# Performance work log

Measured on AMD Instinct MI355X. Metric: run time of the kernel, lower is better.

The kernel has to match this reference:

```python
import jax, jax.numpy as jnp
import numpy as np

DIM = 256
HEADS = 8

def conv1x1(x, W, b):
    # x: [b,c,h,w], W: [o,c], b: [o]
    return jnp.einsum('oc,bchw->bohw', W, x) + b[None, :, None, None]

def setup_inputs() -> dict:
    key = jax.random.key(0)
    ks = jax.random.split(key, 16)
    B, C, H, Wd = 8, DIM, 96, 96
    s = 1.0 / np.sqrt(C)
    inp = {
        'x': jax.random.normal(ks[0], (B, C, H, Wd), jnp.float32),
        'y': jax.random.normal(ks[1], (B, C, H, Wd), jnp.float32),
        'z': jax.random.normal(ks[2], (B, C, H, Wd), jnp.float32),
        'W_qr': jax.random.normal(ks[3], (C // 2, C), jnp.float32) * s,
        'b_qr': jnp.zeros((C // 2,), jnp.float32),
        'W_qd': jax.random.normal(ks[4], (C // 2, C), jnp.float32) * s,
        'b_qd': jnp.zeros((C // 2,), jnp.float32),
        'W_kf': jax.random.normal(ks[5], (C, C), jnp.float32) * s,
        'b_kf': jnp.zeros((C,), jnp.float32),
        'W_vf': jax.random.normal(ks[6], (C, C), jnp.float32) * s,
        'b_vf': jnp.zeros((C,), jnp.float32),
        'W_cat': jax.random.normal(ks[7], (C, C), jnp.float32) * s,
        'b_cat': jnp.zeros((C,), jnp.float32),
        'W_proj': jax.random.normal(ks[8], (C, C), jnp.float32) * s,
        'b_proj': jnp.zeros((C,), jnp.float32),
        'temperature': jnp.ones((HEADS, 1, 1), jnp.float32),
    }
    return inp

def reference(x, y, z, W_qr, b_qr, W_qd, b_qd, W_kf, b_kf, W_vf, b_vf,
              W_cat, b_cat, W_proj, b_proj, temperature):
    b, c, h, w = x.shape
    hw = h * w
    ch = c // HEADS  # channels per head

    q_r = conv1x1(x, W_qr, b_qr)
    q_d = conv1x1(y, W_qd, b_qd)
    k_f = conv1x1(z, W_kf, b_kf)
    v_f = conv1x1(z, W_vf, b_vf)
    q = conv1x1(jnp.concatenate([q_r, q_d], axis=1), W_cat, b_cat)

    def to_heads(t):  # [b, head*ch, h, w] -> [b, head, ch, hw]
        return t.reshape(b, HEADS, ch, hw)

    q = to_heads(q)
    k = to_heads(k_f)
    v = to_heads(v_f)

    # L2-normalize along spatial axis (eps=1e-12 as in F.normalize)
    q = q / jnp.maximum(jnp.linalg.norm(q, axis=-1, keepdims=True), 1e-12)
    k = k / jnp.maximum(jnp.linalg.norm(k, axis=-1, keepdims=True), 1e-12)

    # channel attention: [b,head,ch,ch]
    attn = jnp.einsum('bhcn,bhdn->bhcd', q, k) * temperature[None]
    attn = jax.nn.softmax(attn, axis=-1)
    out = jnp.einsum('bhcd,bhdn->bhcn', attn, v)  # [b,head,ch,hw]
    out = out.reshape(b, c, h, w)
    return conv1x1(out, W_proj, b_proj) + z
```

## Files before the change

### kernel.cpp

```cpp
#include <hip/hip_runtime.h>

#define HW 9216
#define CDIM 256
#define NBATCH 8
#define NHEADS 8

typedef __bf16 bf16x8 __attribute__((ext_vector_type(8)));
typedef float f32x4 __attribute__((ext_vector_type(4)));
typedef float f32x2 __attribute__((ext_vector_type(2)));
typedef unsigned short us4v __attribute__((ext_vector_type(4)));
typedef unsigned short us2v __attribute__((ext_vector_type(2)));
typedef unsigned int u32x4 __attribute__((ext_vector_type(4)));

__device__ inline unsigned short f2bf(float f) {
    unsigned int u = __builtin_bit_cast(unsigned int, f);
    u = (u + 0x7FFF + ((u >> 16) & 1)) >> 16;
    return (unsigned short)u;
}
__device__ inline float bf2f(unsigned short s) {
    unsigned int u = ((unsigned int)s) << 16;
    return __builtin_bit_cast(float, u);
}
__device__ inline unsigned int pk2(float a, float b) {
    return (unsigned int)f2bf(a) | ((unsigned int)f2bf(b) << 16);
}
__device__ inline void stx(float* p, float v) { *p = v; }
__device__ inline void stx(unsigned short* p, float v) { *p = f2bf(v); }

__global__ void fuse_wq(const float* __restrict__ W_cat, const float* __restrict__ W_qr,
                        const float* __restrict__ W_qd, const float* __restrict__ b_qr,
                        const float* __restrict__ b_qd, const float* __restrict__ b_cat,
                        unsigned short* __restrict__ Wq, float* __restrict__ bq) {
    int o = blockIdx.x;
    int c = threadIdx.x;
    float ax = 0.f, ay = 0.f;
    for (int i = 0; i < 128; ++i) {
        ax += W_cat[o * 256 + i] * W_qr[i * 256 + c];
        ay += W_cat[o * 256 + 128 + i] * W_qd[i * 256 + c];
    }
    Wq[o * 512 + c] = f2bf(ax);
    Wq[o * 512 + 256 + c] = f2bf(ay);
    if (c == 0) {
        float s = b_cat[o];
        for (int i = 0; i < 128; ++i)
            s += W_cat[o * 256 + i] * b_qr[i] + W_cat[o * 256 + 128 + i] * b_qd[i];
        bq[o] = s;
    }
}

__global__ void cvt_w(const float* __restrict__ a, const float* __restrict__ b,
                      unsigned short* __restrict__ oa, unsigned short* __restrict__ ob) {
    int i = blockIdx.x * 256 + threadIdx.x;
    oa[i] = f2bf(a[i]);
    ob[i] = f2bf(b[i]);
}

template <int BN, bool DUAL, typename TX, typename TOut>
__global__ __launch_bounds__(256, 2) void gemm2(
    const unsigned short* __restrict__ A0, const unsigned short* __restrict__ A1,
    int a_bs, int Ktot,
    const TX* __restrict__ X0, const TX* __restrict__ X1,
    const float* __restrict__ bias0, const float* __restrict__ bias1,
    const float* __restrict__ resid, TOut* __restrict__ O0, TOut* __restrict__ O1) {
    constexpr int NJ = BN / 32;
    constexpr int NLD = (BN == 128) ? 4 : 2;
    constexpr int BUFB = 8 * BN * 16;

    const int b = blockIdx.z;
    const int n0 = blockIdx.x * BN;
    const int m0 = blockIdx.y * 128;
    const int tid = threadIdx.x;
    const int lane = tid & 63;
    const int wid = tid >> 6;
    const int wm = (wid >> 1) * 64;
    const int wn = (wid & 1) * (BN / 2);
    const int l15 = lane & 15;
    const int quad = lane >> 4;

    __shared__ __align__(16) char Bs[2][BUFB];

    const unsigned short* Ab0 = A0 + (size_t)b * a_bs;
    const unsigned short* Ab1 = DUAL ? A1 : nullptr;
    const TX* Xb0 = X0 + (size_t)b * CDIM * HW;
    const TX* Xb1 = X1 ? X1 + (size_t)b * CDIM * HW : nullptr;

    const int sn = (tid & 31) * NLD;
    const int so = (tid >> 5) * 8;

    f32x4 acc0[4][NJ] = {};
    f32x4 acc1[DUAL ? 4 : 1][NJ] = {};
    float f[8][NLD];

    auto LOADS = [&](int kg) {
        const TX* Xp = (Xb1 && kg >= 256) ? Xb1 : Xb0;
        const int kr = kg & 255;
#pragma unroll
        for (int r = 0; r < 8; ++r) {
            const TX* p = Xp + (size_t)(kr + so + r) * HW + n0 + sn;
            if constexpr (sizeof(TX) == 4) {
                if constexpr (NLD == 4) {
                    f32x4 v = *(const f32x4*)p;
#pragma unroll
                    for (int j = 0; j < 4; ++j) f[r][j] = v[j];
                } else {
                    f32x2 v = *(const f32x2*)p;
                    f[r][0] = v[0]; f[r][1] = v[1];
                }
            } else {
                if constexpr (NLD == 4) {
                    us4v v = *(const us4v*)p;
#pragma unroll
                    for (int j = 0; j < 4; ++j) f[r][j] = bf2f(v[j]);
                } else {
                    us2v v = *(const us2v*)p;
                    f[r][0] = bf2f(v[0]); f[r][1] = bf2f(v[1]);
                }
            }
        }
    };

    auto PKW = [&](int buf) {
        char* base = &Bs[buf][0];
#pragma unroll
        for (int j = 0; j < NLD; ++j) {
            int n = sn + j;
            u32x4 w;
            w[0] = pk2(f[0][j], f[1][j]);
            w[1] = pk2(f[2][j], f[3][j]);
            w[2] = pk2(f[4][j], f[5][j]);
            w[3] = pk2(f[6][j], f[7][j]);
            *(u32x4*)(base + ((((so >> 3) * BN + n) * 16) ^ ((n & 0x38) << 1))) = w;
        }
    };

    auto COMPUTE = [&](int buf, int k0) {
        const char* base = &Bs[buf][0];
#pragma unroll
        for (int kk = 0; kk < 64; kk += 32) {
            bf16x8 bfr[NJ];
#pragma unroll
            for (int nj = 0; nj < NJ; ++nj) {
                int n = wn + nj * 16 + l15;
                bfr[nj] = *(const bf16x8*)(base +
                    (((((kk >> 3) + quad) * BN + n) * 16) ^ ((n & 0x38) << 1)));
            }
            bf16x8 af[4];
#pragma unroll
            for (int mi = 0; mi < 4; ++mi)
                af[mi] = *(const bf16x8*)(Ab0 + (size_t)(m0 + wm + mi * 16 + l15) * Ktot +
                                          k0 + kk + quad * 8);
#pragma unroll
            for (int mi = 0; mi < 4; ++mi)
#pragma unroll
                for (int nj = 0; nj < NJ; ++nj)
                    acc0[mi][nj] = __builtin_amdgcn_mfma_f32_16x16x32_bf16(af[mi], bfr[nj],
                                                                           acc0[mi][nj], 0, 0, 0);
            if constexpr (DUAL) {
#pragma unroll
                for (int mi = 0; mi < 4; ++mi)
                    af[mi] = *(const bf16x8*)(Ab1 + (size_t)(m0 + wm + mi * 16 + l15) * Ktot +
                                              k0 + kk + quad * 8);
#pragma unroll
                for (int mi = 0; mi < 4; ++mi)
#pragma unroll
                    for (int nj = 0; nj < NJ; ++nj)
                        acc1[mi][nj] = __builtin_amdgcn_mfma_f32_16x16x32_bf16(af[mi], bfr[nj],
                                                                               acc1[mi][nj], 0, 0, 0);
            }
        }
    };

    const int nt = Ktot >> 6;
    LOADS(0);
    PKW(0);
    for (int t = 0; t < nt - 1; ++t) {
        LOADS((t + 1) << 6);
        __syncthreads();
        COMPUTE(t & 1, t << 6);
        PKW((t + 1) & 1);
    }
    __syncthreads();
    COMPUTE((nt - 1) & 1, (nt - 1) << 6);

#pragma unroll
    for (int mi = 0; mi < 4; ++mi) {
#pragma unroll
        for (int r = 0; r < 4; ++r) {
            int m = m0 + wm + mi * 16 + quad * 4 + r;
            float bv = bias0[m];
#pragma unroll
            for (int nj = 0; nj < NJ; ++nj) {
                int n = n0 + wn + nj * 16 + l15;
                size_t off = ((size_t)b * CDIM + m) * HW + n;
                float v = acc0[mi][nj][r] + bv;
                if (resid) v += resid[off];
                stx(&O0[off], v);
            }
        }
    }
    if constexpr (DUAL) {
#pragma unroll
        for (int mi = 0; mi < 4; ++mi) {
#pragma unroll
            for (int r = 0; r < 4; ++r) {
                int m = m0 + wm + mi * 16 + quad * 4 + r;
                float bv = bias1[m];
#pragma unroll
                for (int nj = 0; nj < NJ; ++nj) {
                    int n = n0 + wn + nj * 16 + l15;
                    size_t off = ((size_t)b * CDIM + m) * HW + n;
                    stx(&O1[off], acc1[mi][nj][r] + bv);
                }
            }
        }
    }
}

__global__ __launch_bounds__(256) void gram_kernel(
    const unsigned short* __restrict__ q, const unsigned short* __restrict__ k,
    float* __restrict__ G, float* __restrict__ sqq, float* __restrict__ sqk) {
    const int nc = blockIdx.x;
    const int h = blockIdx.y, b = blockIdx.z;
    const int t = threadIdx.x;

    __shared__ float qs[32][128];
    __shared__ float ks[32][129];

    size_t base = ((size_t)b * CDIM + h * 32) * HW + nc * 128;
#pragma unroll
    for (int i = 0; i < 4; ++i) {
        int idx = i * 256 + t;
        int row = idx >> 5, c4 = (idx & 31) * 4;
        us4v qv = *(const us4v*)(q + base + (size_t)row * HW + c4);
        us4v kv = *(const us4v*)(k + base + (size_t)row * HW + c4);
#pragma unroll
        for (int j = 0; j < 4; ++j) {
            qs[row][c4 + j] = bf2f(qv[j]);
            ks[row][c4 + j] = bf2f(kv[j]);
        }
    }
    __syncthreads();

    const int d = t & 31;
    const int cb = t >> 5;
    float acc[4] = {0.f, 0.f, 0.f, 0.f};
    for (int n = 0; n < 128; ++n) {
        float kv = ks[d][n];
#pragma unroll
        for (int p = 0; p < 4; ++p) acc[p] += qs[cb + 8 * p][n] * kv;
    }

    float* Gp = G + (size_t)(b * 8 + h) * 32 * 32;
#pragma unroll
    for (int p = 0; p < 4; ++p) atomicAdd(&Gp[(cb + 8 * p) * 32 + d], acc[p]);

    if (t < 64) {
        int c = t & 31;
        float sq = 0.f;
        if (t < 32) {
            for (int n = 0; n < 128; ++n) { float v = qs[c][n]; sq += v * v; }
            atomicAdd(&sqq[(b * 8 + h) * 32 + c], sq);
        } else {
            for (int n = 0; n < 128; ++n) { float v = ks[c][n]; sq += v * v; }
            atomicAdd(&sqk[(b * 8 + h) * 32 + c], sq);
        }
    }
}

__global__ __launch_bounds__(1024) void softmax_kernel(
    const float* __restrict__ G, const float* __restrict__ sqq,
    const float* __restrict__ sqk, const float* __restrict__ temp,
    float* __restrict__ A) {
    int bh = blockIdx.x;
    int h = bh & 7;
    int c = threadIdx.y, d = threadIdx.x;
    float nq = fmaxf(sqrtf(sqq[bh * 32 + c]), 1e-12f);
    float nk = fmaxf(sqrtf(sqk[bh * 32 + d]), 1e-12f);
    float v = G[(size_t)(bh * 32 + c) * 32 + d] / (nq * nk) * temp[h];
    float m = v;
    for (int s = 16; s > 0; s >>= 1) m = fmaxf(m, __shfl_xor(m, s, 32));
    float e = __expf(v - m);
    float sum = e;
    for (int s = 16; s > 0; s >>= 1) sum += __shfl_xor(sum, s, 32);
    A[(size_t)(bh * 32 + c) * 32 + d] = e / sum;
}

__global__ __launch_bounds__(256) void build_m(const float* __restrict__ W_proj,
                                               const float* __restrict__ A,
                                               unsigned short* __restrict__ M) {
    int o = blockIdx.x;
    int b = blockIdx.y;
    int t = threadIdx.x;
    int h = t >> 5, d = t & 31;
    const float* Ab = A + (size_t)(b * 8 + h) * 32 * 32;
    float acc = 0.f;
    for (int c = 0; c < 32; ++c)
        acc += W_proj[o * 256 + h * 32 + c] * Ab[c * 32 + d];
    M[((size_t)b * 256 + o) * 256 + t] = f2bf(acc);
}

extern "C" void kernel_launch(void* const* d_in, const int* in_sizes, int n_in,
                              void* d_out, int out_size, void* d_ws, size_t ws_size,
                              hipStream_t stream) {
    const float* x = (const float*)d_in[0];
    const float* y = (const float*)d_in[1];
    const float* z = (const float*)d_in[2];
    const float* W_qr = (const float*)d_in[3];
    const float* b_qr = (const float*)d_in[4];
    const float* W_qd = (const float*)d_in[5];
    const float* b_qd = (const float*)d_in[6];
    const float* W_kf = (const float*)d_in[7];
    const float* b_kf = (const float*)d_in[8];
    const float* W_vf = (const float*)d_in[9];
    const float* b_vf = (const float*)d_in[10];
    const float* W_cat = (const float*)d_in[11];
    const float* b_cat = (const float*)d_in[12];
    const float* W_proj = (const float*)d_in[13];
    const float* b_proj = (const float*)d_in[14];
    const float* temp = (const float*)d_in[15];
    float* out = (float*)d_out;

    char* ws = (char*)d_ws;
    const size_t NT = (size_t)NBATCH * CDIM * HW;
    unsigned short* qb = (unsigned short*)ws;
    unsigned short* kb = qb + NT;
    unsigned short* vb = kb + NT;
    char* p = (char*)(vb + NT);
    unsigned short* Wq = (unsigned short*)p;  p += 256 * 512 * 2;
    unsigned short* Wk = (unsigned short*)p;  p += 256 * 256 * 2;
    unsigned short* Wv = (unsigned short*)p;  p += 256 * 256 * 2;
    float* bq  = (float*)p;                   p += 1024;
    float* G   = (float*)p;                   p += 64 * 32 * 32 * 4;
    float* sqq = (float*)p;                   p += 2048 * 4;
    float* sqk = (float*)p;                   p += 2048 * 4;
    float* Aat = (float*)p;                   p += 64 * 32 * 32 * 4;
    unsigned short* Mb = (unsigned short*)p;  p += (size_t)8 * 256 * 256 * 2;

    hipMemsetAsync(G, 0, 262144 + 8192 + 8192, stream);

    fuse_wq<<<256, 256, 0, stream>>>(W_cat, W_qr, W_qd, b_qr, b_qd, b_cat, Wq, bq);
    cvt_w<<<256, 256, 0, stream>>>(W_kf, W_vf, Wk, Wv);

    gemm2<128, false, float, unsigned short><<<dim3(HW / 128, 2, NBATCH), 256, 0, stream>>>(
        Wq, nullptr, 0, 512, x, y, bq, nullptr, nullptr, qb, nullptr);
    gemm2<64, true, float, unsigned short><<<dim3(HW / 64, 2, NBATCH), 256, 0, stream>>>(
        Wk, Wv, 0, 256, z, nullptr, b_kf, b_vf, nullptr, kb, vb);

    gram_kernel<<<dim3(HW / 128, NHEADS, NBATCH), 256, 0, stream>>>(qb, kb, G, sqq, sqk);
    softmax_kernel<<<64, dim3(32, 32), 0, stream>>>(G, sqq, sqk, temp, Aat);
    build_m<<<dim3(256, 8), 256, 0, stream>>>(W_proj, Aat, Mb);

    gemm2<128, false, unsigned short, float><<<dim3(HW / 128, 2, NBATCH), 256, 0, stream>>>(
        Mb, nullptr, 256 * 256, 256, vb, nullptr, b_proj, nullptr, z, out, nullptr);
}
```

Baseline: 567.4 us.

## Compute Gram matrix with MFMA partials and drop atomics; restructure GEMM sync

Replaces the scalar shared-memory Gram kernel with an MFMA 32x32x16 bf16 kernel. Each block covers a 1024-column chunk for one batch-head and writes deterministic partial sums instead of issuing atomics. The softmax kernel now reduces the 9 partials, which removes the memset. The GEMM main loop also moves its barrier to after the LDS write and adds a scheduling barrier, so only one sync runs per iteration. The Gram grid is small (576 blocks), which may limit occupancy, and reading 64-bit-strided rows directly from global memory could be less coalesced.

```diff
diff --git a/kernel.cpp b/kernel.cpp
--- a/kernel.cpp
+++ b/kernel.cpp
@@ -4,12 +4,15 @@
 #define CDIM 256
 #define NBATCH 8
 #define NHEADS 8
+#define GCH 9
 
 typedef __bf16 bf16x8 __attribute__((ext_vector_type(8)));
 typedef float f32x4 __attribute__((ext_vector_type(4)));
 typedef float f32x2 __attribute__((ext_vector_type(2)));
+typedef float f32x16 __attribute__((ext_vector_type(16)));
+typedef unsigned short us2v __attribute__((ext_vector_type(2)));
 typedef unsigned short us4v __attribute__((ext_vector_type(4)));
-typedef unsigned short us2v __attribute__((ext_vector_type(2)));
+typedef unsigned short us8v __attribute__((ext_vector_type(8)));
 typedef unsigned int u32x4 __attribute__((ext_vector_type(4)));
 
 __device__ inline unsigned short f2bf(float f) {
@@ -173,13 +176,14 @@
     const int nt = Ktot >> 6;
     LOADS(0);
     PKW(0);
+    __syncthreads();
     for (int t = 0; t < nt - 1; ++t) {
         LOADS((t + 1) << 6);
-        __syncthreads();
+        __builtin_amdgcn_sched_barrier(0);
         COMPUTE(t & 1, t << 6);
         PKW((t + 1) & 1);
-    }
-    __syncthreads();
+        __syncthreads();
+    }
     COMPUTE((nt - 1) & 1, (nt - 1) << 6);
 
 #pragma unroll
@@ -216,67 +220,81 @@
     }
 }
 
-__global__ __launch_bounds__(256) void gram_kernel(
+__global__ __launch_bounds__(256) void gram_mfma(
     const unsigned short* __restrict__ q, const unsigned short* __restrict__ k,
-    float* __restrict__ G, float* __restrict__ sqq, float* __restrict__ sqk) {
-    const int nc = blockIdx.x;
-    const int h = blockIdx.y, b = blockIdx.z;
+    float* __restrict__ Gp, float* __restrict__ sqp, float* __restrict__ skp) {
+    const int ch = blockIdx.x;
+    const int bh = blockIdx.y;
     const int t = threadIdx.x;
-
-    __shared__ float qs[32][128];
-    __shared__ float ks[32][129];
-
-    size_t base = ((size_t)b * CDIM + h * 32) * HW + nc * 128;
-#pragma unroll
-    for (int i = 0; i < 4; ++i) {
-        int idx = i * 256 + t;
-        int row = idx >> 5, c4 = (idx & 31) * 4;
-        us4v qv = *(const us4v*)(q + base + (size_t)row * HW + c4);
-        us4v kv = *(const us4v*)(k + base + (size_t)row * HW + c4);
-#pragma unroll
-        for (int j = 0; j < 4; ++j) {
-            qs[row][c4 + j] = bf2f(qv[j]);
-            ks[row][c4 + j] = bf2f(kv[j]);
-        }
+    const int lane = t & 63, w = t >> 6;
+    const int row = lane & 31, half = lane >> 5;
+
+    const size_t rb = ((size_t)bh * 32 + row) * HW + ch * 1024 + w * 256 + half * 8;
+    const unsigned short* qp = q + rb;
+    const unsigned short* kp = k + rb;
+
+    f32x16 acc = {};
+    float sq = 0.f, sk = 0.f;
+#pragma unroll
+    for (int n = 0; n < 256; n += 16) {
+        us8v rq = *(const us8v*)(qp + n);
+        us8v rk = *(const us8v*)(kp + n);
+        bf16x8 aq = __builtin_bit_cast(bf16x8, rq);
+        bf16x8 ak = __builtin_bit_cast(bf16x8, rk);
+        acc = __builtin_amdgcn_mfma_f32_32x32x16_bf16(aq, ak, acc, 0, 0, 0);
+#pragma unroll
+        for (int j = 0; j < 8; ++j) {
+            float fq = bf2f(rq[j]);
+            float fk = bf2f(rk[j]);
+            sq += fq * fq;
+            sk += fk * fk;
+        }
+    }
+    sq += __shfl_xor(sq, 32, 64);
+    sk += __shfl_xor(sk, 32, 64);
+
+    __shared__ float gs[4][1024];
+    __shared__ float sqs[4][32];
+    __shared__ float sks[4][32];
+    if (half == 0) { sqs[w][row] = sq; sks[w][row] = sk; }
+#pragma unroll
+    for (int r = 0; r < 16; ++r) {
+        int cr = (r & 3) + 8 * (r >> 2) + 4 * half;
+        gs[w][cr * 32 + row] = acc[r];
     }
     __syncthreads();
 
-    const int d = t & 31;
-    const int cb = t >> 5;
-    float acc[4] = {0.f, 0.f, 0.f, 0.f};
-    for (int n = 0; n < 128; ++n) {
-        float kv = ks[d][n];
-#pragma unroll
-        for (int p = 0; p < 4; ++p) acc[p] += qs[cb + 8 * p][n] * kv;
-    }
-
-    float* Gp = G + (size_t)(b * 8 + h) * 32 * 32;
-#pragma unroll
-    for (int p = 0; p < 4; ++p) atomicAdd(&Gp[(cb + 8 * p) * 32 + d], acc[p]);
-
-    if (t < 64) {
-        int c = t & 31;
-        float sq = 0.f;
-        if (t < 32) {
-            for (int n = 0; n < 128; ++n) { float v = qs[c][n]; sq += v * v; }
-            atomicAdd(&sqq[(b * 8 + h) * 32 + c], sq);
-        } else {
-            for (int n = 0; n < 128; ++n) { float v = ks[c][n]; sq += v * v; }
-            atomicAdd(&sqk[(b * 8 + h) * 32 + c], sq);
-        }
+    float* Gpo = Gp + ((size_t)ch * 64 + bh) * 1024;
+#pragma unroll
+    for (int j = 0; j < 4; ++j) {
+        int idx = j * 256 + t;
+        Gpo[idx] = gs[0][idx] + gs[1][idx] + gs[2][idx] + gs[3][idx];
+    }
+    if (t < 32)
+        sqp[((size_t)ch * 64 + bh) * 32 + t] = sqs[0][t] + sqs[1][t] + sqs[2][t] + sqs[3][t];
+    else if (t < 64) {
+        int c = t - 32;
+        skp[((size_t)ch * 64 + bh) * 32 + c] = sks[0][c] + sks[1][c] + sks[2][c] + sks[3][c];
     }
 }
 
 __global__ __launch_bounds__(1024) void softmax_kernel(
-    const float* __restrict__ G, const float* __restrict__ sqq,
-    const float* __restrict__ sqk, const float* __restrict__ temp,
+    const float* __restrict__ Gp, const float* __restrict__ sqp,
+    const float* __restrict__ skp, const float* __restrict__ temp,
     float* __restrict__ A) {
     int bh = blockIdx.x;
     int h = bh & 7;
     int c = threadIdx.y, d = threadIdx.x;
-    float nq = fmaxf(sqrtf(sqq[bh * 32 + c]), 1e-12f);
-    float nk = fmaxf(sqrtf(sqk[bh * 32 + d]), 1e-12f);
-    float v = G[(size_t)(bh * 32 + c) * 32 + d] / (nq * nk) * temp[h];
+    float g = 0.f, qq = 0.f, kk = 0.f;
+#pragma unroll
+    for (int ch = 0; ch < GCH; ++ch) {
+        g += Gp[((size_t)ch * 64 + bh) * 1024 + c * 32 + d];
+        qq += sqp[((size_t)ch * 64 + bh) * 32 + c];
+        kk += skp[((size_t)ch * 64 + bh) * 32 + d];
+    }
+    float nq = fmaxf(sqrtf(qq), 1e-12f);
+    float nk = fmaxf(sqrtf(kk), 1e-12f);
+    float v = g / (nq * nk) * temp[h];
     float m = v;
     for (int s = 16; s > 0; s >>= 1) m = fmaxf(m, __shfl_xor(m, s, 32));
     float e = __expf(v - m);
@@ -330,13 +348,11 @@
     unsigned short* Wk = (unsigned short*)p;  p += 256 * 256 * 2;
     unsigned short* Wv = (unsigned short*)p;  p += 256 * 256 * 2;
     float* bq  = (float*)p;                   p += 1024;
-    float* G   = (float*)p;                   p += 64 * 32 * 32 * 4;
-    float* sqq = (float*)p;                   p += 2048 * 4;
-    float* sqk = (float*)p;                   p += 2048 * 4;
+    float* Gp  = (float*)p;                   p += (size_t)GCH * 64 * 1024 * 4;
+    float* sqp = (float*)p;                   p += GCH * 64 * 32 * 4;
+    float* skp = (float*)p;                   p += GCH * 64 * 32 * 4;
     float* Aat = (float*)p;                   p += 64 * 32 * 32 * 4;
     unsigned short* Mb = (unsigned short*)p;  p += (size_t)8 * 256 * 256 * 2;
-
-    hipMemsetAsync(G, 0, 262144 + 8192 + 8192, stream);
 
     fuse_wq<<<256, 256, 0, stream>>>(W_cat, W_qr, W_qd, b_qr, b_qd, b_cat, Wq, bq);
     cvt_w<<<256, 256, 0, stream>>>(W_kf, W_vf, Wk, Wv);
@@ -346,8 +362,8 @@
     gemm2<64, true, float, unsigned short><<<dim3(HW / 64, 2, NBATCH), 256, 0, stream>>>(
         Wk, Wv, 0, 256, z, nullptr, b_kf, b_vf, nullptr, kb, vb);
 
-    gram_kernel<<<dim3(HW / 128, NHEADS, NBATCH), 256, 0, stream>>>(qb, kb, G, sqq, sqk);
-    softmax_kernel<<<64, dim3(32, 32), 0, stream>>>(G, sqq, sqk, temp, Aat);
+    gram_mfma<<<dim3(GCH, 64), 256, 0, stream>>>(qb, kb, Gp, sqp, skp);
+    softmax_kernel<<<64, dim3(32, 32), 0, stream>>>(Gp, sqp, skp, temp, Aat);
     build_m<<<dim3(256, 8), 256, 0, stream>>>(W_proj, Aat, Mb);
 
     gemm2<128, false, unsigned short, float><<<dim3(HW / 128, 2, NBATCH), 256, 0, stream>>>(
```

Result: faster. 517.6 us (-8.8%).
